# Optimization experiments

Hardware: AMD Instinct MI355X
Metric: run time of the kernel (lower is better)

The kernel has to match this reference:

```python
import jax, jax.numpy as jnp
import numpy as np

H = 256
V = 50257
L = 2048
B = 32


def setup_inputs() -> dict:
    key = jax.random.key(0)
    ks = jax.random.split(key, 14)
    s = 0.05  # weight scale
    return {
        "tokens": jax.random.randint(ks[0], (B,), 0, V),
        "hidden": jax.random.normal(ks[1], (1, B, H), jnp.float32),
        "cell": jax.random.normal(ks[2], (1, B, H), jnp.float32),
        "encoder_outputs": jax.random.normal(ks[3], (B, L, H), jnp.float32),
        "emb_table": jax.random.normal(ks[4], (V, H), jnp.float32) * s,
        "W_attn": jax.random.normal(ks[5], (H, 2 * H), jnp.float32) * s,
        "b_attn": jax.random.normal(ks[6], (H,), jnp.float32) * s,
        "v": jax.random.normal(ks[7], (H,), jnp.float32) * s,
        "W_ih": jax.random.normal(ks[8], (4 * H, 2 * H), jnp.float32) * s,
        "b_ih": jax.random.normal(ks[9], (4 * H,), jnp.float32) * s,
        "W_hh": jax.random.normal(ks[10], (4 * H, H), jnp.float32) * s,
        "b_hh": jax.random.normal(ks[11], (4 * H,), jnp.float32) * s,
        "W_out": jax.random.normal(ks[12], (V, 2 * H), jnp.float32) * s,
        "b_out": jax.random.normal(ks[13], (V,), jnp.float32) * s,
    }


def reference(tokens, hidden, cell, encoder_outputs, emb_table, W_attn, b_attn, v,
              W_ih, b_ih, W_hh, b_hh, W_out, b_out):
    # embedded: (B, H); dropout is identity in eval mode
    embedded = emb_table[tokens]
    h_last = hidden[-1]  # (B, H)

    # Bahdanau-style energy: attn(cat(h, e)) then dot with v (NO tanh, per source)
    # split the 2H-input linear into hidden part and encoder part
    Wh, We = W_attn[:, :H], W_attn[:, H:]
    eh = h_last @ Wh.T                                      # (B, H)
    ee = jnp.einsum('blh,kh->blk', encoder_outputs, We)     # (B, L, H)
    energy = eh[:, None, :] + ee + b_attn                   # (B, L, H)
    scores = energy @ v                                     # (B, L)
    attn_weights = jax.nn.softmax(scores, axis=-1)          # (B, L)

    # context = bmm(attn_weights, encoder_outputs)
    attn_applied = jnp.einsum('bl,blh->bh', attn_weights, encoder_outputs)  # (B, H)

    # single-step LSTM, input = cat(embedded, context): (B, 2H)
    x = jnp.concatenate([embedded, attn_applied], axis=-1)
    gates = x @ W_ih.T + b_ih + hidden[0] @ W_hh.T + b_hh   # (B, 4H)
    i_g, f_g, g_g, o_g = jnp.split(gates, 4, axis=-1)
    c_new = jax.nn.sigmoid(f_g) * cell[0] + jax.nn.sigmoid(i_g) * jnp.tanh(g_g)
    h_new = jax.nn.sigmoid(o_g) * jnp.tanh(c_new)           # (B, H)

    # output projection on cat(lstm_out, context): (B, 2H) -> (B, V)
    logits = jnp.concatenate([h_new, attn_applied], axis=-1) @ W_out.T + b_out
    log_probs = jax.nn.log_softmax(logits, axis=-1)

    return (log_probs, h_new[None], c_new[None], attn_weights[:, None, :])
```

## Files before the change

kernel.cpp:

```cpp
#include <hip/hip_runtime.h>
#include <cstddef>

#define H   256
#define L   2048
#define B   32
#define V   50257
#define H2  512
#define H4  1024
#define CH  64
#define NCH (L/CH)

#define LP_OFF 0
#define HN_OFF (B*V)
#define CN_OFF (HN_OFF + B*H)
#define AW_OFF (CN_OFF + B*H)

#define WS_XL    0
#define WS_S     (WS_XL + B*H2)
#define WS_AV    (WS_S + B*L)
#define WS_AM    (WS_AV + B*NCH*H)
#define WS_AZ    (WS_AM + B*NCH)
#define WS_PM    (WS_AZ + B*NCH)
#define WS_PZ    (WS_PM + 12800)

#define NBLK_LOG 393

typedef __attribute__((ext_vector_type(8))) short bf16x8;
typedef __attribute__((ext_vector_type(4))) float f32x4;

__device__ inline unsigned short f2bf(float f) {
    unsigned u = __builtin_bit_cast(unsigned, f);
    u += 0x7FFFu + ((u >> 16) & 1u);
    return (unsigned short)(u >> 16);
}

__global__ __launch_bounds__(256) void k_attn(const float* __restrict__ W_attn,
                                              const float* __restrict__ v,
                                              const float* __restrict__ enc,
                                              float* __restrict__ ws) {
    int bid = blockIdx.x;
    int b = bid >> 5, chunk = bid & (NCH - 1);
    int t = threadIdx.x;
    int wave = t >> 6, lane = t & 63;
    int g = lane >> 4, u = lane & 15;
    __shared__ float v_s[H];
    __shared__ float w_s[H];
    __shared__ float s_lds[CH];
    __shared__ float p_lds[CH];
    __shared__ float red[CH];
    __shared__ float vec_lds[4][256];

    v_s[t] = v[t];
    __syncthreads();
    {
        const float* base = W_attn + H + t;
        float wa = 0.f, wb = 0.f;
        #pragma unroll 8
        for (int k = 0; k < H; k += 2) {
            wa += v_s[k]     * base[(size_t)k * H2];
            wb += v_s[k + 1] * base[(size_t)(k + 1) * H2];
        }
        w_s[t] = wa + wb;
    }
    __syncthreads();

    size_t rowbase = (size_t)b * L + chunk * CH;
    const float4* w4s = (const float4*)w_s;
    float4 w0 = w4s[u], w1 = w4s[16 + u], w2 = w4s[32 + u], w3 = w4s[48 + u];

    #pragma unroll
    for (int ir = 0; ir < 4; ir++) {
        int rl = wave * 16 + ir * 4 + g;
        const float4* e4 = (const float4*)(enc + (rowbase + rl) * H);
        float4 a0 = e4[u], a1 = e4[16 + u], a2 = e4[32 + u], a3 = e4[48 + u];
        float p = a0.x * w0.x + a0.y * w0.y + a0.z * w0.z + a0.w * w0.w
                + a1.x * w1.x + a1.y * w1.y + a1.z * w1.z + a1.w * w1.w
                + a2.x * w2.x + a2.y * w2.y + a2.z * w2.z + a2.w * w2.w
                + a3.x * w3.x + a3.y * w3.y + a3.z * w3.z + a3.w * w3.w;
        p += __shfl_down(p, 8); p += __shfl_down(p, 4);
        p += __shfl_down(p, 2); p += __shfl_down(p, 1);
        if (u == 0) s_lds[rl] = p;
    }
    __syncthreads();

    if (t < CH) red[t] = s_lds[t];
    __syncthreads();
    for (int off = 32; off; off >>= 1) { if (t < off) red[t] = fmaxf(red[t], red[t + off]); __syncthreads(); }
    float m = red[0];
    __syncthreads();
    if (t < CH) {
        float e = __expf(s_lds[t] - m);
        p_lds[t] = e; red[t] = e;
        ws[WS_S + rowbase + t] = s_lds[t];
    }
    __syncthreads();
    for (int off = 32; off; off >>= 1) { if (t < off) red[t] += red[t + off]; __syncthreads(); }

    float4 acc = make_float4(0.f, 0.f, 0.f, 0.f);
    const float4* ebase = (const float4*)(enc + (rowbase + wave * 16) * H);
    #pragma unroll 4
    for (int i = 0; i < 16; i++) {
        float p = p_lds[wave * 16 + i];
        float4 a = ebase[i * 64 + lane];
        acc.x += p * a.x; acc.y += p * a.y; acc.z += p * a.z; acc.w += p * a.w;
    }
    *(float4*)&vec_lds[wave][lane * 4] = acc;
    __syncthreads();
    ws[WS_AV + (size_t)bid * 256 + t] = vec_lds[0][t] + vec_lds[1][t] + vec_lds[2][t] + vec_lds[3][t];
    if (t == 0) { ws[WS_AM + bid] = m; ws[WS_AZ + bid] = red[0]; }
}

__global__ __launch_bounds__(256) void k_fuse(const int* __restrict__ tokens,
                                              const float* __restrict__ emb,
                                              const float* __restrict__ hidden,
                                              const float* __restrict__ cell,
                                              const float* __restrict__ W_ih,
                                              const float* __restrict__ b_ih,
                                              const float* __restrict__ W_hh,
                                              const float* __restrict__ b_hh,
                                              float* __restrict__ ws,
                                              float* __restrict__ out) {
    int blk = blockIdx.x;
    int b = blk >> 4, s = blk & 15;
    int t = threadIdx.x;
    int wave = t >> 6, lane = t & 63;
    __shared__ float mc[NCH], zc[NCH];
    __shared__ float xs[H2];
    __shared__ float hs[H];
    __shared__ float gl[64];

    if (t < NCH) { mc[t] = ws[WS_AM + b * NCH + t]; zc[t] = ws[WS_AZ + b * NCH + t]; }
    hs[t] = hidden[(size_t)b * H + t];
    int tok = tokens[b];
    xs[t] = emb[(size_t)tok * H + t];
    __syncthreads();

    float M = -1e30f;
    #pragma unroll
    for (int c = 0; c < NCH; c++) M = fmaxf(M, mc[c]);
    float Z = 0.f;
    #pragma unroll
    for (int c = 0; c < NCH; c++) Z += zc[c] * __expf(mc[c] - M);
    float inv = 1.f / Z;
    float acc = 0.f;
    #pragma unroll 8
    for (int c = 0; c < NCH; c++) acc += __expf(mc[c] - M) * ws[WS_AV + (size_t)(b * NCH + c) * H + t];
    acc *= inv;
    xs[H + t] = acc;
    if (s == 0) {
        ws[WS_XL + b * H2 + H + t] = acc;
        #pragma unroll
        for (int j = 0; j < 8; j++) {
            int l = t + 256 * j;
            out[AW_OFF + (size_t)b * L + l] = __expf(ws[WS_S + (size_t)b * L + l] - M) * inv;
        }
    }
    __syncthreads();

    int ts = s * 16;
    const float4* xs4 = (const float4*)xs;
    const float4* hs4 = (const float4*)hs;
    float4 x0 = xs4[lane * 2], x1 = xs4[lane * 2 + 1];
    float4 xh = hs4[lane];
    for (int it = 0; it < 16; it++) {
        int j = (wave << 8) + ts + it;
        const float4* wi = (const float4*)(W_ih + (size_t)j * H2);
        float4 a0 = wi[lane * 2], a1 = wi[lane * 2 + 1];
        const float4* wh = (const float4*)(W_hh + (size_t)j * H);
        float4 a2 = wh[lane];
        float p = a0.x * x0.x + a0.y * x0.y + a0.z * x0.z + a0.w * x0.w
                + a1.x * x1.x + a1.y * x1.y + a1.z * x1.z + a1.w * x1.w
                + a2.x * xh.x + a2.y * xh.y + a2.z * xh.z + a2.w * xh.w;
        #pragma unroll
        for (int off = 32; off; off >>= 1) p += __shfl_down(p, off);
        if (lane == 0) gl[wave * 16 + it] = p + b_ih[j] + b_hh[j];
    }
    __syncthreads();

    if (t < 16) {
        int tt = ts + t;
        float ig = gl[t], fg = gl[16 + t], gg = gl[32 + t], og = gl[48 + t];
        float c = cell[(size_t)b * H + tt];
        float si = 1.f / (1.f + expf(-ig));
        float sf = 1.f / (1.f + expf(-fg));
        float so = 1.f / (1.f + expf(-og));
        float cn = sf * c + si * tanhf(gg);
        float hn = so * tanhf(cn);
        out[HN_OFF + b * H + tt] = hn;
        out[CN_OFF + b * H + tt] = cn;
        ws[WS_XL + b * H2 + tt] = hn;
    }
}

__global__ __launch_bounds__(256) void k_logits(const float* __restrict__ W_out,
                                                const float* __restrict__ b_out,
                                                float* __restrict__ ws,
                                                float* __restrict__ out) {
    __shared__ unsigned short Xl[32 * 520];
    int t = threadIdx.x;
    const float4* xl4 = (const float4*)(ws + WS_XL);
    #pragma unroll
    for (int it = 0; it < 16; it++) {
        int fi = t + 256 * it;
        int b = fi >> 7, kq = fi & 127;
        float4 xv = xl4[b * 128 + kq];
        unsigned p0 = (unsigned)f2bf(xv.x) | ((unsigned)f2bf(xv.y) << 16);
        unsigned p1 = (unsigned)f2bf(xv.z) | ((unsigned)f2bf(xv.w) << 16);
        unsigned* dst = (unsigned*)&Xl[b * 520 + kq * 4];
        dst[0] = p0; dst[1] = p1;
    }
    __syncthreads();

    int wave = t >> 6, lane = t & 63, quad = lane >> 4, m = lane & 15;
    int rbase = blockIdx.x * 128 + wave * 32;
    f32x4 zero4 = {0.f, 0.f, 0.f, 0.f};
    f32x4 acc[2][2];
    acc[0][0] = zero4; acc[0][1] = zero4; acc[1][0] = zero4; acc[1][1] = zero4;

    int r0 = rbase + m;
    int r1 = rbase + 16 + m;
    int r0c = r0 < V ? r0 : V - 1;
    int r1c = r1 < V ? r1 : V - 1;
    const float* wp0 = W_out + (size_t)r0c * H2 + quad * 8;
    const float* wp1 = W_out + (size_t)r1c * H2 + quad * 8;

    for (int kp = 0; kp < 16; kp++) {
        int k0 = kp * 32;
        float4 lo0 = *(const float4*)(wp0 + k0);
        float4 hi0 = *(const float4*)(wp0 + k0 + 4);
        float4 lo1 = *(const float4*)(wp1 + k0);
        float4 hi1 = *(const float4*)(wp1 + k0 + 4);
        bf16x8 a0, a1;
        a0[0]=(short)f2bf(lo0.x); a0[1]=(short)f2bf(lo0.y); a0[2]=(short)f2bf(lo0.z); a0[3]=(short)f2bf(lo0.w);
        a0[4]=(short)f2bf(hi0.x); a0[5]=(short)f2bf(hi0.y); a0[6]=(short)f2bf(hi0.z); a0[7]=(short)f2bf(hi0.w);
        a1[0]=(short)f2bf(lo1.x); a1[1]=(short)f2bf(lo1.y); a1[2]=(short)f2bf(lo1.z); a1[3]=(short)f2bf(lo1.w);
        a1[4]=(short)f2bf(hi1.x); a1[5]=(short)f2bf(hi1.y); a1[6]=(short)f2bf(hi1.z); a1[7]=(short)f2bf(hi1.w);
        bf16x8 b0 = *(bf16x8*)&Xl[(size_t)m * 520 + k0 + quad * 8];
        bf16x8 b1 = *(bf16x8*)&Xl[(size_t)(16 + m) * 520 + k0 + quad * 8];
        acc[0][0] = __builtin_amdgcn_mfma_f32_16x16x32_bf16(a0, b0, acc[0][0], 0, 0, 0);
        acc[0][1] = __builtin_amdgcn_mfma_f32_16x16x32_bf16(a0, b1, acc[0][1], 0, 0, 0);
        acc[1][0] = __builtin_amdgcn_mfma_f32_16x16x32_bf16(a1, b0, acc[1][0], 0, 0, 0);
        acc[1][1] = __builtin_amdgcn_mfma_f32_16x16x32_bf16(a1, b1, acc[1][1], 0, 0, 0);
    }

    float val[2][2][4];
    #pragma unroll
    for (int s = 0; s < 2; s++) {
        #pragma unroll
        for (int i = 0; i < 4; i++) {
            int rr = rbase + s * 16 + quad * 4 + i;
            float bo = (rr < V) ? b_out[rr] : 0.f;
            #pragma unroll
            for (int nt = 0; nt < 2; nt++) {
                float vv = acc[s][nt][i] + bo;
                if (rr < V) {
                    int bcol = nt * 16 + m;
                    out[(size_t)bcol * V + rr] = vv;
                    val[s][nt][i] = vv;
                } else {
                    val[s][nt][i] = -1e30f;
                }
            }
        }
    }
    float pm[2], pz[2];
    #pragma unroll
    for (int nt = 0; nt < 2; nt++) {
        float mx = -1e30f;
        #pragma unroll
        for (int s = 0; s < 2; s++)
            #pragma unroll
            for (int i = 0; i < 4; i++) mx = fmaxf(mx, val[s][nt][i]);
        float sm = 0.f;
        #pragma unroll
        for (int s = 0; s < 2; s++)
            #pragma unroll
            for (int i = 0; i < 4; i++) sm += __expf(val[s][nt][i] - mx);
        pm[nt] = mx; pz[nt] = sm;
    }
    #pragma unroll
    for (int off = 16; off <= 32; off <<= 1) {
        #pragma unroll
        for (int nt = 0; nt < 2; nt++) {
            float om = __shfl_xor(pm[nt], off);
            float oz = __shfl_xor(pz[nt], off);
            float nm = fmaxf(pm[nt], om);
            pz[nt] = pz[nt] * __expf(pm[nt] - nm) + oz * __expf(om - nm);
            pm[nt] = nm;
        }
    }
    __syncthreads();
    float* red = (float*)Xl;
    if (quad == 0) {
        #pragma unroll
        for (int nt = 0; nt < 2; nt++) {
            red[wave * 32 + nt * 16 + m]       = pm[nt];
            red[128 + wave * 32 + nt * 16 + m] = pz[nt];
        }
    }
    __syncthreads();
    if (t < 32) {
        float mf = -1e30f;
        #pragma unroll
        for (int w = 0; w < 4; w++) mf = fmaxf(mf, red[w * 32 + t]);
        float z = 0.f;
        #pragma unroll
        for (int w = 0; w < 4; w++) z += red[128 + w * 32 + t] * __expf(red[w * 32 + t] - mf);
        ws[WS_PM + t * 400 + blockIdx.x] = mf;
        ws[WS_PZ + t * 400 + blockIdx.x] = z;
    }
}

__global__ __launch_bounds__(256) void k_lsm_final(const float* __restrict__ ws,
                                                   float* __restrict__ out) {
    int b = blockIdx.y, t = threadIdx.x;
    __shared__ float rm[256], rz[256];
    float m = -1e30f, z = 0.f;
    for (int i = t; i < NBLK_LOG; i += 256) {
        float mi = ws[WS_PM + b * 400 + i];
        float zi = ws[WS_PZ + b * 400 + i];
        float nm = fmaxf(m, mi);
        z = z * __expf(m - nm) + zi * __expf(mi - nm);
        m = nm;
    }
    rm[t] = m; rz[t] = z; __syncthreads();
    for (int off = 128; off; off >>= 1) {
        if (t < off) {
            float m2 = rm[t + off], z2 = rz[t + off];
            float nm = fmaxf(rm[t], m2);
            rz[t] = rz[t] * __expf(rm[t] - nm) + z2 * __expf(m2 - nm);
            rm[t] = nm;
        }
        __syncthreads();
    }
    float M = rm[0], LZ = logf(rz[0]);
    int rbase = blockIdx.x * 1024 + t;
    #pragma unroll
    for (int j = 0; j < 4; j++) {
        int r = rbase + 256 * j;
        if (r < V) {
            size_t i = (size_t)b * V + r;
            out[i] = out[i] - M - LZ;
        }
    }
}

extern "C" void kernel_launch(void* const* d_in, const int* in_sizes, int n_in,
                              void* d_out, int out_size, void* d_ws, size_t ws_size,
                              hipStream_t stream) {
    const int*   tokens = (const int*)d_in[0];
    const float* hidden = (const float*)d_in[1];
    const float* cell   = (const float*)d_in[2];
    const float* enc    = (const float*)d_in[3];
    const float* emb    = (const float*)d_in[4];
    const float* W_attn = (const float*)d_in[5];
    const float* v      = (const float*)d_in[7];
    const float* W_ih   = (const float*)d_in[8];
    const float* b_ih   = (const float*)d_in[9];
    const float* W_hh   = (const float*)d_in[10];
    const float* b_hh   = (const float*)d_in[11];
    const float* W_out  = (const float*)d_in[12];
    const float* b_out  = (const float*)d_in[13];
    float* out = (float*)d_out;
    float* ws  = (float*)d_ws;

    k_attn<<<B * NCH, 256, 0, stream>>>(W_attn, v, enc, ws);
    k_fuse<<<B * 16, 256, 0, stream>>>(tokens, emb, hidden, cell, W_ih, b_ih, W_hh, b_hh, ws, out);
    k_logits<<<NBLK_LOG, 256, 0, stream>>>(W_out, b_out, ws, out);
    k_lsm_final<<<dim3((V + 1023) / 1024, B), 256, 0, stream>>>(ws, out);
}
```

Measured before the change: 297.2 us.

## Merge four kernels into one cooperative persistent kernel with grid syncs

Replaces the separate attention, LSTM, logits and log-softmax kernels with a single cooperative kernel of 512 blocks that runs each phase and separates them with grid.sync. Work is remapped so each block handles multiple attention chunks and logits tiles (now 64-row tiles with a one-step software prefetch of W_out). The goal is to remove per-launch overhead and inter-kernel gaps, at the cost of grid-wide barrier latency and reduced per-phase parallelism. A fallback launches the same kernel four times if the cooperative launch fails.

```diff
diff --git a/kernel.cpp b/kernel.cpp
--- a/kernel.cpp
+++ b/kernel.cpp
@@ -1,5 +1,8 @@
 #include <hip/hip_runtime.h>
+#include <hip/hip_cooperative_groups.h>
 #include <cstddef>
+
+namespace cg = cooperative_groups;
 
 #define H   256
 #define L   2048
@@ -21,9 +24,10 @@
 #define WS_AM    (WS_AV + B*NCH*H)
 #define WS_AZ    (WS_AM + B*NCH)
 #define WS_PM    (WS_AZ + B*NCH)
-#define WS_PZ    (WS_PM + 12800)
-
-#define NBLK_LOG 393
+#define WS_PZ    (WS_PM + 32*800)
+
+#define NT_LOG 786
+#define NBLK   512
 
 typedef __attribute__((ext_vector_type(8))) short bf16x8;
 typedef __attribute__((ext_vector_type(4))) float f32x4;
@@ -34,313 +38,302 @@
     return (unsigned short)(u >> 16);
 }
 
-__global__ __launch_bounds__(256) void k_attn(const float* __restrict__ W_attn,
-                                              const float* __restrict__ v,
-                                              const float* __restrict__ enc,
-                                              float* __restrict__ ws) {
-    int bid = blockIdx.x;
-    int b = bid >> 5, chunk = bid & (NCH - 1);
-    int t = threadIdx.x;
+__global__ __launch_bounds__(256, 2) void k_mega(
+    int p_lo, int p_hi,
+    const int*   __restrict__ tokens, const float* __restrict__ emb,
+    const float* __restrict__ hidden, const float* __restrict__ cell,
+    const float* __restrict__ enc,    const float* __restrict__ W_attn,
+    const float* __restrict__ v,      const float* __restrict__ W_ih,
+    const float* __restrict__ b_ih,   const float* __restrict__ W_hh,
+    const float* __restrict__ b_hh,   const float* __restrict__ W_out,
+    const float* __restrict__ b_out,  float* __restrict__ ws,
+    float* __restrict__ out)
+{
+    __shared__ __align__(16) float smf[8576];
+    cg::grid_group grid = cg::this_grid();
+    int blk = blockIdx.x, t = threadIdx.x;
     int wave = t >> 6, lane = t & 63;
-    int g = lane >> 4, u = lane & 15;
-    __shared__ float v_s[H];
-    __shared__ float w_s[H];
-    __shared__ float s_lds[CH];
-    __shared__ float p_lds[CH];
-    __shared__ float red[CH];
-    __shared__ float vec_lds[4][256];
-
-    v_s[t] = v[t];
-    __syncthreads();
-    {
-        const float* base = W_attn + H + t;
-        float wa = 0.f, wb = 0.f;
+
+    if (p_lo <= 0 && 0 <= p_hi) {
+        float* v_s   = smf;
+        float* w_s   = smf + 256;
+        float* s_lds = smf + 512;
+        float* p_lds = smf + 576;
+        float* red   = smf + 640;
+        float* vec   = smf + 704;
+        int g = lane >> 4, u = lane & 15;
+
+        v_s[t] = v[t];
+        __syncthreads();
+        {
+            const float* base = W_attn + H + t;
+            float wa = 0.f, wb = 0.f;
+            #pragma unroll 8
+            for (int k = 0; k < H; k += 2) {
+                wa += v_s[k]     * base[(size_t)k * H2];
+                wb += v_s[k + 1] * base[(size_t)(k + 1) * H2];
+            }
+            w_s[t] = wa + wb;
+        }
+        __syncthreads();
+        const float4* w4s = (const float4*)w_s;
+        float4 w0 = w4s[u], w1 = w4s[16 + u], w2 = w4s[32 + u], w3 = w4s[48 + u];
+
+        for (int pass = 0; pass < 2; pass++) {
+            int bid = blk + pass * NBLK;
+            int b = bid >> 5, chunk = bid & (NCH - 1);
+            size_t rowbase = (size_t)b * L + chunk * CH;
+
+            #pragma unroll
+            for (int ir = 0; ir < 4; ir++) {
+                int rl = wave * 16 + ir * 4 + g;
+                const float4* e4 = (const float4*)(enc + (rowbase + rl) * H);
+                float4 a0 = e4[u], a1 = e4[16 + u], a2 = e4[32 + u], a3 = e4[48 + u];
+                float p = a0.x * w0.x + a0.y * w0.y + a0.z * w0.z + a0.w * w0.w
+                        + a1.x * w1.x + a1.y * w1.y + a1.z * w1.z + a1.w * w1.w
+                        + a2.x * w2.x + a2.y * w2.y + a2.z * w2.z + a2.w * w2.w
+                        + a3.x * w3.x + a3.y * w3.y + a3.z * w3.z + a3.w * w3.w;
+                p += __shfl_down(p, 8); p += __shfl_down(p, 4);
+                p += __shfl_down(p, 2); p += __shfl_down(p, 1);
+                if (u == 0) s_lds[rl] = p;
+            }
+            __syncthreads();
+
+            if (t < CH) red[t] = s_lds[t];
+            __syncthreads();
+            for (int off = 32; off; off >>= 1) { if (t < off) red[t] = fmaxf(red[t], red[t + off]); __syncthreads(); }
+            float m = red[0];
+            __syncthreads();
+            if (t < CH) {
+                float e = __expf(s_lds[t] - m);
+                p_lds[t] = e; red[t] = e;
+                ws[WS_S + rowbase + t] = s_lds[t];
+            }
+            __syncthreads();
+            for (int off = 32; off; off >>= 1) { if (t < off) red[t] += red[t + off]; __syncthreads(); }
+
+            float4 acc = make_float4(0.f, 0.f, 0.f, 0.f);
+            const float4* ebase = (const float4*)(enc + (rowbase + wave * 16) * H);
+            #pragma unroll 4
+            for (int i = 0; i < 16; i++) {
+                float p = p_lds[wave * 16 + i];
+                float4 a = ebase[i * 64 + lane];
+                acc.x += p * a.x; acc.y += p * a.y; acc.z += p * a.z; acc.w += p * a.w;
+            }
+            *(float4*)&vec[wave * 256 + lane * 4] = acc;
+            __syncthreads();
+            ws[WS_AV + (size_t)bid * 256 + t] = vec[t] + vec[256 + t] + vec[512 + t] + vec[768 + t];
+            if (t == 0) { ws[WS_AM + bid] = m; ws[WS_AZ + bid] = red[0]; }
+            __syncthreads();
+        }
+    }
+    if (p_lo <= 0 && 1 <= p_hi) grid.sync();
+
+    if (p_lo <= 1 && 1 <= p_hi) {
+        int b = blk >> 4, s = blk & 15;
+        float* mc = smf;
+        float* zc = smf + 32;
+        float* xs = smf + 64;
+        float* hs = smf + 576;
+        float* gl = smf + 832;
+
+        if (t < NCH) { mc[t] = ws[WS_AM + b * NCH + t]; zc[t] = ws[WS_AZ + b * NCH + t]; }
+        hs[t] = hidden[(size_t)b * H + t];
+        xs[t] = emb[(size_t)tokens[b] * H + t];
+        __syncthreads();
+
+        float M = -1e30f;
+        #pragma unroll
+        for (int c = 0; c < NCH; c++) M = fmaxf(M, mc[c]);
+        float Z = 0.f;
+        #pragma unroll
+        for (int c = 0; c < NCH; c++) Z += zc[c] * __expf(mc[c] - M);
+        float inv = 1.f / Z;
+        float acc = 0.f;
         #pragma unroll 8
-        for (int k = 0; k < H; k += 2) {
-            wa += v_s[k]     * base[(size_t)k * H2];
-            wb += v_s[k + 1] * base[(size_t)(k + 1) * H2];
-        }
-        w_s[t] = wa + wb;
-    }
-    __syncthreads();
-
-    size_t rowbase = (size_t)b * L + chunk * CH;
-    const float4* w4s = (const float4*)w_s;
-    float4 w0 = w4s[u], w1 = w4s[16 + u], w2 = w4s[32 + u], w3 = w4s[48 + u];
-
-    #pragma unroll
-    for (int ir = 0; ir < 4; ir++) {
-        int rl = wave * 16 + ir * 4 + g;
-        const float4* e4 = (const float4*)(enc + (rowbase + rl) * H);
-        float4 a0 = e4[u], a1 = e4[16 + u], a2 = e4[32 + u], a3 = e4[48 + u];
-        float p = a0.x * w0.x + a0.y * w0.y + a0.z * w0.z + a0.w * w0.w
-                + a1.x * w1.x + a1.y * w1.y + a1.z * w1.z + a1.w * w1.w
-                + a2.x * w2.x + a2.y * w2.y + a2.z * w2.z + a2.w * w2.w
-                + a3.x * w3.x + a3.y * w3.y + a3.z * w3.z + a3.w * w3.w;
-        p += __shfl_down(p, 8); p += __shfl_down(p, 4);
-        p += __shfl_down(p, 2); p += __shfl_down(p, 1);
-        if (u == 0) s_lds[rl] = p;
-    }
-    __syncthreads();
-
-    if (t < CH) red[t] = s_lds[t];
-    __syncthreads();
-    for (int off = 32; off; off >>= 1) { if (t < off) red[t] = fmaxf(red[t], red[t + off]); __syncthreads(); }
-    float m = red[0];
-    __syncthreads();
-    if (t < CH) {
-        float e = __expf(s_lds[t] - m);
-        p_lds[t] = e; red[t] = e;
-        ws[WS_S + rowbase + t] = s_lds[t];
-    }
-    __syncthreads();
-    for (int off = 32; off; off >>= 1) { if (t < off) red[t] += red[t + off]; __syncthreads(); }
-
-    float4 acc = make_float4(0.f, 0.f, 0.f, 0.f);
-    const float4* ebase = (const float4*)(enc + (rowbase + wave * 16) * H);
-    #pragma unroll 4
-    for (int i = 0; i < 16; i++) {
-        float p = p_lds[wave * 16 + i];
-        float4 a = ebase[i * 64 + lane];
-        acc.x += p * a.x; acc.y += p * a.y; acc.z += p * a.z; acc.w += p * a.w;
-    }
-    *(float4*)&vec_lds[wave][lane * 4] = acc;
-    __syncthreads();
-    ws[WS_AV + (size_t)bid * 256 + t] = vec_lds[0][t] + vec_lds[1][t] + vec_lds[2][t] + vec_lds[3][t];
-    if (t == 0) { ws[WS_AM + bid] = m; ws[WS_AZ + bid] = red[0]; }
-}
-
-__global__ __launch_bounds__(256) void k_fuse(const int* __restrict__ tokens,
-                                              const float* __restrict__ emb,
-                                              const float* __restrict__ hidden,
-                                              const float* __restrict__ cell,
-                                              const float* __restrict__ W_ih,
-                                              const float* __restrict__ b_ih,
-                                              const float* __restrict__ W_hh,
-                                              const float* __restrict__ b_hh,
-                                              float* __restrict__ ws,
-                                              float* __restrict__ out) {
-    int blk = blockIdx.x;
-    int b = blk >> 4, s = blk & 15;
-    int t = threadIdx.x;
-    int wave = t >> 6, lane = t & 63;
-    __shared__ float mc[NCH], zc[NCH];
-    __shared__ float xs[H2];
-    __shared__ float hs[H];
-    __shared__ float gl[64];
-
-    if (t < NCH) { mc[t] = ws[WS_AM + b * NCH + t]; zc[t] = ws[WS_AZ + b * NCH + t]; }
-    hs[t] = hidden[(size_t)b * H + t];
-    int tok = tokens[b];
-    xs[t] = emb[(size_t)tok * H + t];
-    __syncthreads();
-
-    float M = -1e30f;
-    #pragma unroll
-    for (int c = 0; c < NCH; c++) M = fmaxf(M, mc[c]);
-    float Z = 0.f;
-    #pragma unroll
-    for (int c = 0; c < NCH; c++) Z += zc[c] * __expf(mc[c] - M);
-    float inv = 1.f / Z;
-    float acc = 0.f;
-    #pragma unroll 8
-    for (int c = 0; c < NCH; c++) acc += __expf(mc[c] - M) * ws[WS_AV + (size_t)(b * NCH + c) * H + t];
-    acc *= inv;
-    xs[H + t] = acc;
-    if (s == 0) {
-        ws[WS_XL + b * H2 + H + t] = acc;
+        for (int c = 0; c < NCH; c++) acc += __expf(mc[c] - M) * ws[WS_AV + (size_t)(b * NCH + c) * H + t];
+        acc *= inv;
+        xs[H + t] = acc;
+        if (s == 0) {
+            ws[WS_XL + b * H2 + H + t] = acc;
+            #pragma unroll
+            for (int j = 0; j < 8; j++) {
+                int l = t + 256 * j;
+                out[AW_OFF + (size_t)b * L + l] = __expf(ws[WS_S + (size_t)b * L + l] - M) * inv;
+            }
+        }
+        __syncthreads();
+
+        int ts = s * 16;
+        const float4* xs4 = (const float4*)xs;
+        const float4* hs4 = (const float4*)hs;
+        float4 x0 = xs4[lane * 2], x1 = xs4[lane * 2 + 1];
+        float4 xh = hs4[lane];
+        for (int it = 0; it < 16; it++) {
+            int j = (wave << 8) + ts + it;
+            const float4* wi = (const float4*)(W_ih + (size_t)j * H2);
+            float4 a0 = wi[lane * 2], a1 = wi[lane * 2 + 1];
+            const float4* wh = (const float4*)(W_hh + (size_t)j * H);
+            float4 a2 = wh[lane];
+            float p = a0.x * x0.x + a0.y * x0.y + a0.z * x0.z + a0.w * x0.w
+                    + a1.x * x1.x + a1.y * x1.y + a1.z * x1.z + a1.w * x1.w
+                    + a2.x * xh.x + a2.y * xh.y + a2.z * xh.z + a2.w * xh.w;
+            #pragma unroll
+            for (int off = 32; off; off >>= 1) p += __shfl_down(p, off);
+            if (lane == 0) gl[wave * 16 + it] = p + b_ih[j] + b_hh[j];
+        }
+        __syncthreads();
+
+        if (t < 16) {
+            int tt = ts + t;
+            float ig = gl[t], fg = gl[16 + t], gg = gl[32 + t], og = gl[48 + t];
+            float c = cell[(size_t)b * H + tt];
+            float si = 1.f / (1.f + expf(-ig));
+            float sf = 1.f / (1.f + expf(-fg));
+            float so = 1.f / (1.f + expf(-og));
+            float cn = sf * c + si * tanhf(gg);
+            float hn = so * tanhf(cn);
+            out[HN_OFF + b * H + tt] = hn;
+            out[CN_OFF + b * H + tt] = cn;
+            ws[WS_XL + b * H2 + tt] = hn;
+        }
+    }
+    if (p_lo <= 1 && 2 <= p_hi) grid.sync();
+
+    if (p_lo <= 2 && 2 <= p_hi) {
+        unsigned short* Xl = (unsigned short*)smf;
+        float* red2 = smf + 8320;
+        const float4* xl4 = (const float4*)(ws + WS_XL);
         #pragma unroll
-        for (int j = 0; j < 8; j++) {
-            int l = t + 256 * j;
-            out[AW_OFF + (size_t)b * L + l] = __expf(ws[WS_S + (size_t)b * L + l] - M) * inv;
-        }
-    }
-    __syncthreads();
-
-    int ts = s * 16;
-    const float4* xs4 = (const float4*)xs;
-    const float4* hs4 = (const float4*)hs;
-    float4 x0 = xs4[lane * 2], x1 = xs4[lane * 2 + 1];
-    float4 xh = hs4[lane];
-    for (int it = 0; it < 16; it++) {
-        int j = (wave << 8) + ts + it;
-        const float4* wi = (const float4*)(W_ih + (size_t)j * H2);
-        float4 a0 = wi[lane * 2], a1 = wi[lane * 2 + 1];
-        const float4* wh = (const float4*)(W_hh + (size_t)j * H);
-        float4 a2 = wh[lane];
-        float p = a0.x * x0.x + a0.y * x0.y + a0.z * x0.z + a0.w * x0.w
-                + a1.x * x1.x + a1.y * x1.y + a1.z * x1.z + a1.w * x1.w
-                + a2.x * xh.x + a2.y * xh.y + a2.z * xh.z + a2.w * xh.w;
-        #pragma unroll
-        for (int off = 32; off; off >>= 1) p += __shfl_down(p, off);
-        if (lane == 0) gl[wave * 16 + it] = p + b_ih[j] + b_hh[j];
-    }
-    __syncthreads();
-
-    if (t < 16) {
-        int tt = ts + t;
-        float ig = gl[t], fg = gl[16 + t], gg = gl[32 + t], og = gl[48 + t];
-        float c = cell[(size_t)b * H + tt];
-        float si = 1.f / (1.f + expf(-ig));
-        float sf = 1.f / (1.f + expf(-fg));
-        float so = 1.f / (1.f + expf(-og));
-        float cn = sf * c + si * tanhf(gg);
-        float hn = so * tanhf(cn);
-        out[HN_OFF + b * H + tt] = hn;
-        out[CN_OFF + b * H + tt] = cn;
-        ws[WS_XL + b * H2 + tt] = hn;
-    }
-}
-
-__global__ __launch_bounds__(256) void k_logits(const float* __restrict__ W_out,
-                                                const float* __restrict__ b_out,
-                                                float* __restrict__ ws,
-                                                float* __restrict__ out) {
-    __shared__ unsigned short Xl[32 * 520];
-    int t = threadIdx.x;
-    const float4* xl4 = (const float4*)(ws + WS_XL);
-    #pragma unroll
-    for (int it = 0; it < 16; it++) {
-        int fi = t + 256 * it;
-        int b = fi >> 7, kq = fi & 127;
-        float4 xv = xl4[b * 128 + kq];
-        unsigned p0 = (unsigned)f2bf(xv.x) | ((unsigned)f2bf(xv.y) << 16);
-        unsigned p1 = (unsigned)f2bf(xv.z) | ((unsigned)f2bf(xv.w) << 16);
-        unsigned* dst = (unsigned*)&Xl[b * 520 + kq * 4];
-        dst[0] = p0; dst[1] = p1;
-    }
-    __syncthreads();
-
-    int wave = t >> 6, lane = t & 63, quad = lane >> 4, m = lane & 15;
-    int rbase = blockIdx.x * 128 + wave * 32;
-    f32x4 zero4 = {0.f, 0.f, 0.f, 0.f};
-    f32x4 acc[2][2];
-    acc[0][0] = zero4; acc[0][1] = zero4; acc[1][0] = zero4; acc[1][1] = zero4;
-
-    int r0 = rbase + m;
-    int r1 = rbase + 16 + m;
-    int r0c = r0 < V ? r0 : V - 1;
-    int r1c = r1 < V ? r1 : V - 1;
-    const float* wp0 = W_out + (size_t)r0c * H2 + quad * 8;
-    const float* wp1 = W_out + (size_t)r1c * H2 + quad * 8;
-
-    for (int kp = 0; kp < 16; kp++) {
-        int k0 = kp * 32;
-        float4 lo0 = *(const float4*)(wp0 + k0);
-        float4 hi0 = *(const float4*)(wp0 + k0 + 4);
-        float4 lo1 = *(const float4*)(wp1 + k0);
-        float4 hi1 = *(const float4*)(wp1 + k0 + 4);
-        bf16x8 a0, a1;
-        a0[0]=(short)f2bf(lo0.x); a0[1]=(short)f2bf(lo0.y); a0[2]=(short)f2bf(lo0.z); a0[3]=(short)f2bf(lo0.w);
-        a0[4]=(short)f2bf(hi0.x); a0[5]=(short)f2bf(hi0.y); a0[6]=(short)f2bf(hi0.z); a0[7]=(short)f2bf(hi0.w);
-        a1[0]=(short)f2bf(lo1.x); a1[1]=(short)f2bf(lo1.y); a1[2]=(short)f2bf(lo1.z); a1[3]=(short)f2bf(lo1.w);
-        a1[4]=(short)f2bf(hi1.x); a1[5]=(short)f2bf(hi1.y); a1[6]=(short)f2bf(hi1.z); a1[7]=(short)f2bf(hi1.w);
-        bf16x8 b0 = *(bf16x8*)&Xl[(size_t)m * 520 + k0 + quad * 8];
-        bf16x8 b1 = *(bf16x8*)&Xl[(size_t)(16 + m) * 520 + k0 + quad * 8];
-        acc[0][0] = __builtin_amdgcn_mfma_f32_16x16x32_bf16(a0, b0, acc[0][0], 0, 0, 0);
-        acc[0][1] = __builtin_amdgcn_mfma_f32_16x16x32_bf16(a0, b1, acc[0][1], 0, 0, 0);
-        acc[1][0] = __builtin_amdgcn_mfma_f32_16x16x32_bf16(a1, b0, acc[1][0], 0, 0, 0);
-        acc[1][1] = __builtin_amdgcn_mfma_f32_16x16x32_bf16(a1, b1, acc[1][1], 0, 0, 0);
-    }
-
-    float val[2][2][4];
-    #pragma unroll
-    for (int s = 0; s < 2; s++) {
-        #pragma unroll
-        for (int i = 0; i < 4; i++) {
-            int rr = rbase + s * 16 + quad * 4 + i;
-            float bo = (rr < V) ? b_out[rr] : 0.f;
+        for (int it = 0; it < 16; it++) {
+            int fi = t + 256 * it;
+            int bb = fi >> 7, kq = fi & 127;
+            float4 xv = xl4[bb * 128 + kq];
+            unsigned p0 = (unsigned)f2bf(xv.x) | ((unsigned)f2bf(xv.y) << 16);
+            unsigned p1 = (unsigned)f2bf(xv.z) | ((unsigned)f2bf(xv.w) << 16);
+            unsigned* dst = (unsigned*)&Xl[bb * 520 + kq * 4];
+            dst[0] = p0; dst[1] = p1;
+        }
+        __syncthreads();
+
+        int quad = lane >> 4, m = lane & 15;
+        for (int tile = blk; tile < NT_LOG; tile += NBLK) {
+            int rbase = tile * 64 + wave * 16;
+            int r0 = rbase + m;
+            int rc = r0 < V ? r0 : V - 1;
+            const float* wp = W_out + (size_t)rc * H2 + quad * 8;
+            f32x4 acc0 = {0.f, 0.f, 0.f, 0.f}, acc1 = {0.f, 0.f, 0.f, 0.f};
+
+            float4 lo = *(const float4*)(wp);
+            float4 hi = *(const float4*)(wp + 4);
+            #pragma unroll
+            for (int kp = 0; kp < 16; kp++) {
+                int k0 = kp * 32;
+                float4 nlo, nhi;
+                if (kp < 15) {
+                    nlo = *(const float4*)(wp + k0 + 32);
+                    nhi = *(const float4*)(wp + k0 + 36);
+                }
+                bf16x8 a;
+                a[0]=(short)f2bf(lo.x); a[1]=(short)f2bf(lo.y); a[2]=(short)f2bf(lo.z); a[3]=(short)f2bf(lo.w);
+                a[4]=(short)f2bf(hi.x); a[5]=(short)f2bf(hi.y); a[6]=(short)f2bf(hi.z); a[7]=(short)f2bf(hi.w);
+                bf16x8 b0 = *(bf16x8*)&Xl[(size_t)m * 520 + k0 + quad * 8];
+                bf16x8 b1 = *(bf16x8*)&Xl[(size_t)(16 + m) * 520 + k0 + quad * 8];
+                acc0 = __builtin_amdgcn_mfma_f32_16x16x32_bf16(a, b0, acc0, 0, 0, 0);
+                acc1 = __builtin_amdgcn_mfma_f32_16x16x32_bf16(a, b1, acc1, 0, 0, 0);
+                lo = nlo; hi = nhi;
+            }
+
+            float val[2][4];
+            #pragma unroll
+            for (int i = 0; i < 4; i++) {
+                int rr = rbase + quad * 4 + i;
+                float bo = (rr < V) ? b_out[rr] : 0.f;
+                float v0 = acc0[i] + bo, v1 = acc1[i] + bo;
+                if (rr < V) {
+                    out[(size_t)m * V + rr]        = v0;
+                    out[(size_t)(16 + m) * V + rr] = v1;
+                    val[0][i] = v0; val[1][i] = v1;
+                } else { val[0][i] = -1e30f; val[1][i] = -1e30f; }
+            }
+            float pm[2], pz[2];
             #pragma unroll
             for (int nt = 0; nt < 2; nt++) {
-                float vv = acc[s][nt][i] + bo;
-                if (rr < V) {
-                    int bcol = nt * 16 + m;
-                    out[(size_t)bcol * V + rr] = vv;
-                    val[s][nt][i] = vv;
-                } else {
-                    val[s][nt][i] = -1e30f;
-                }
-            }
-        }
-    }
-    float pm[2], pz[2];
-    #pragma unroll
-    for (int nt = 0; nt < 2; nt++) {
-        float mx = -1e30f;
-        #pragma unroll
-        for (int s = 0; s < 2; s++)
-            #pragma unroll
-            for (int i = 0; i < 4; i++) mx = fmaxf(mx, val[s][nt][i]);
-        float sm = 0.f;
-        #pragma unroll
-        for (int s = 0; s < 2; s++)
-            #pragma unroll
-            for (int i = 0; i < 4; i++) sm += __expf(val[s][nt][i] - mx);
-        pm[nt] = mx; pz[nt] = sm;
-    }
-    #pragma unroll
-    for (int off = 16; off <= 32; off <<= 1) {
-        #pragma unroll
-        for (int nt = 0; nt < 2; nt++) {
-            float om = __shfl_xor(pm[nt], off);
-            float oz = __shfl_xor(pz[nt], off);
-            float nm = fmaxf(pm[nt], om);
-            pz[nt] = pz[nt] * __expf(pm[nt] - nm) + oz * __expf(om - nm);
-            pm[nt] = nm;
-        }
-    }
-    __syncthreads();
-    float* red = (float*)Xl;
-    if (quad == 0) {
-        #pragma unroll
-        for (int nt = 0; nt < 2; nt++) {
-            red[wave * 32 + nt * 16 + m]       = pm[nt];
-            red[128 + wave * 32 + nt * 16 + m] = pz[nt];
-        }
-    }
-    __syncthreads();
-    if (t < 32) {
-        float mf = -1e30f;
-        #pragma unroll
-        for (int w = 0; w < 4; w++) mf = fmaxf(mf, red[w * 32 + t]);
-        float z = 0.f;
-        #pragma unroll
-        for (int w = 0; w < 4; w++) z += red[128 + w * 32 + t] * __expf(red[w * 32 + t] - mf);
-        ws[WS_PM + t * 400 + blockIdx.x] = mf;
-        ws[WS_PZ + t * 400 + blockIdx.x] = z;
-    }
-}
-
-__global__ __launch_bounds__(256) void k_lsm_final(const float* __restrict__ ws,
-                                                   float* __restrict__ out) {
-    int b = blockIdx.y, t = threadIdx.x;
-    __shared__ float rm[256], rz[256];
-    float m = -1e30f, z = 0.f;
-    for (int i = t; i < NBLK_LOG; i += 256) {
-        float mi = ws[WS_PM + b * 400 + i];
-        float zi = ws[WS_PZ + b * 400 + i];
-        float nm = fmaxf(m, mi);
-        z = z * __expf(m - nm) + zi * __expf(mi - nm);
-        m = nm;
-    }
-    rm[t] = m; rz[t] = z; __syncthreads();
-    for (int off = 128; off; off >>= 1) {
-        if (t < off) {
-            float m2 = rm[t + off], z2 = rz[t + off];
-            float nm = fmaxf(rm[t], m2);
-            rz[t] = rz[t] * __expf(rm[t] - nm) + z2 * __expf(m2 - nm);
-            rm[t] = nm;
-        }
-        __syncthreads();
-    }
-    float M = rm[0], LZ = logf(rz[0]);
-    int rbase = blockIdx.x * 1024 + t;
-    #pragma unroll
-    for (int j = 0; j < 4; j++) {
-        int r = rbase + 256 * j;
-        if (r < V) {
-            size_t i = (size_t)b * V + r;
-            out[i] = out[i] - M - LZ;
+                float mx = -1e30f;
+                #pragma unroll
+                for (int i = 0; i < 4; i++) mx = fmaxf(mx, val[nt][i]);
+                float sm = 0.f;
+                #pragma unroll
+                for (int i = 0; i < 4; i++) sm += __expf(val[nt][i] - mx);
+                pm[nt] = mx; pz[nt] = sm;
+            }
+            #pragma unroll
+            for (int off = 16; off <= 32; off <<= 1) {
+                #pragma unroll
+                for (int nt = 0; nt < 2; nt++) {
+                    float om = __shfl_xor(pm[nt], off);
+                    float oz = __shfl_xor(pz[nt], off);
+                    float nm = fmaxf(pm[nt], om);
+                    pz[nt] = pz[nt] * __expf(pm[nt] - nm) + oz * __expf(om - nm);
+                    pm[nt] = nm;
+                }
+            }
+            __syncthreads();
+            if (quad == 0) {
+                #pragma unroll
+                for (int nt = 0; nt < 2; nt++) {
+                    red2[wave * 32 + nt * 16 + m]       = pm[nt];
+                    red2[128 + wave * 32 + nt * 16 + m] = pz[nt];
+                }
+            }
+            __syncthreads();
+            if (t < 32) {
+                float mf = -1e30f;
+                #pragma unroll
+                for (int w = 0; w < 4; w++) mf = fmaxf(mf, red2[w * 32 + t]);
+                float z = 0.f;
+                #pragma unroll
+                for (int w = 0; w < 4; w++) z += red2[128 + w * 32 + t] * __expf(red2[w * 32 + t] - mf);
+                ws[WS_PM + t * 800 + tile] = mf;
+                ws[WS_PZ + t * 800 + tile] = z;
+            }
+        }
+    }
+    if (p_lo <= 2 && 3 <= p_hi) grid.sync();
+
+    if (p_lo <= 3 && 3 <= p_hi) {
+        if (blk < 416) {
+            int b = blk / 13, ch = blk - b * 13;
+            float* rm = smf;
+            float* rz = smf + 256;
+            float m = -1e30f, z = 0.f;
+            for (int i = t; i < NT_LOG; i += 256) {
+                float mi = ws[WS_PM + b * 800 + i];
+                float zi = ws[WS_PZ + b * 800 + i];
+                float nm = fmaxf(m, mi);
+                z = z * __expf(m - nm) + zi * __expf(mi - nm);
+                m = nm;
+            }
+            rm[t] = m; rz[t] = z; __syncthreads();
+            for (int off = 128; off; off >>= 1) {
+                if (t < off) {
+                    float m2 = rm[t + off], z2 = rz[t + off];
+                    float nm = fmaxf(rm[t], m2);
+                    rz[t] = rz[t] * __expf(rm[t] - nm) + z2 * __expf(m2 - nm);
+                    rm[t] = nm;
+                }
+                __syncthreads();
+            }
+            float MM = rm[0], LZ = logf(rz[0]);
+            int rb = ch * 4096 + t;
+            #pragma unroll
+            for (int j = 0; j < 16; j++) {
+                int r = rb + 256 * j;
+                if (r < V) {
+                    size_t i = (size_t)b * V + r;
+                    out[i] = out[i] - MM - LZ;
+                }
+            }
         }
     }
 }
@@ -364,8 +357,15 @@
     float* out = (float*)d_out;
     float* ws  = (float*)d_ws;
 
-    k_attn<<<B * NCH, 256, 0, stream>>>(W_attn, v, enc, ws);
-    k_fuse<<<B * 16, 256, 0, stream>>>(tokens, emb, hidden, cell, W_ih, b_ih, W_hh, b_hh, ws, out);
-    k_logits<<<NBLK_LOG, 256, 0, stream>>>(W_out, b_out, ws, out);
-    k_lsm_final<<<dim3((V + 1023) / 1024, B), 256, 0, stream>>>(ws, out);
+    int p_lo = 0, p_hi = 3;
+    void* args[] = { &p_lo, &p_hi, &tokens, &emb, &hidden, &cell, &enc, &W_attn,
+                     &v, &W_ih, &b_ih, &W_hh, &b_hh, &W_out, &b_out, &ws, &out };
+    hipError_t e = hipLaunchCooperativeKernel((const void*)k_mega, dim3(NBLK), dim3(256),
+                                              args, 0, stream);
+    if (e != hipSuccess) {
+        for (int p = 0; p < 4; p++) {
+            k_mega<<<NBLK, 256, 0, stream>>>(p, p, tokens, emb, hidden, cell, enc, W_attn,
+                                             v, W_ih, b_ih, W_hh, b_hh, W_out, b_out, ws, out);
+        }
+    }
 }
```

Result: slower. 489.9 us (+64.8%).

## Halve logits tile per block and software-prefetch W_out rows three steps ahead

Applied to the files above, without the earlier changes.

The logits kernel now gives each wave 16 vocabulary rows instead of 32, which doubles the grid to 786 blocks. A register-level prefetch pipeline loads W_out three k-steps ahead so the bf16 conversion and MFMA overlap with memory latency. It also adds a launch-bounds occupancy hint, a separate LDS reduction buffer, and full unrolling of the attention accumulation loop. The partial-softmax workspace stride widens to match the larger grid, at the cost of more partials for the final reduction and higher register pressure from the prefetch buffers.

```diff
diff --git a/kernel.cpp b/kernel.cpp
--- a/kernel.cpp
+++ b/kernel.cpp
@@ -21,9 +21,9 @@
 #define WS_AM    (WS_AV + B*NCH*H)
 #define WS_AZ    (WS_AM + B*NCH)
 #define WS_PM    (WS_AZ + B*NCH)
-#define WS_PZ    (WS_PM + 12800)
-
-#define NBLK_LOG 393
+#define WS_PZ    (WS_PM + 32*800)
+
+#define NT_LOG 786
 
 typedef __attribute__((ext_vector_type(8))) short bf16x8;
 typedef __attribute__((ext_vector_type(4))) float f32x4;
@@ -98,7 +98,7 @@
 
     float4 acc = make_float4(0.f, 0.f, 0.f, 0.f);
     const float4* ebase = (const float4*)(enc + (rowbase + wave * 16) * H);
-    #pragma unroll 4
+    #pragma unroll
     for (int i = 0; i < 16; i++) {
         float p = p_lds[wave * 16 + i];
         float4 a = ebase[i * 64 + lane];
@@ -131,8 +131,7 @@
 
     if (t < NCH) { mc[t] = ws[WS_AM + b * NCH + t]; zc[t] = ws[WS_AZ + b * NCH + t]; }
     hs[t] = hidden[(size_t)b * H + t];
-    int tok = tokens[b];
-    xs[t] = emb[(size_t)tok * H + t];
+    xs[t] = emb[(size_t)tokens[b] * H + t];
     __syncthreads();
 
     float M = -1e30f;
@@ -192,90 +191,73 @@
     }
 }
 
-__global__ __launch_bounds__(256) void k_logits(const float* __restrict__ W_out,
-                                                const float* __restrict__ b_out,
-                                                float* __restrict__ ws,
-                                                float* __restrict__ out) {
+__global__ __launch_bounds__(256, 4) void k_logits(const float* __restrict__ W_out,
+                                                   const float* __restrict__ b_out,
+                                                   float* __restrict__ ws,
+                                                   float* __restrict__ out) {
     __shared__ unsigned short Xl[32 * 520];
+    __shared__ float red2[256];
     int t = threadIdx.x;
     const float4* xl4 = (const float4*)(ws + WS_XL);
     #pragma unroll
     for (int it = 0; it < 16; it++) {
         int fi = t + 256 * it;
-        int b = fi >> 7, kq = fi & 127;
-        float4 xv = xl4[b * 128 + kq];
+        int bb = fi >> 7, kq = fi & 127;
+        float4 xv = xl4[bb * 128 + kq];
         unsigned p0 = (unsigned)f2bf(xv.x) | ((unsigned)f2bf(xv.y) << 16);
         unsigned p1 = (unsigned)f2bf(xv.z) | ((unsigned)f2bf(xv.w) << 16);
-        unsigned* dst = (unsigned*)&Xl[b * 520 + kq * 4];
+        unsigned* dst = (unsigned*)&Xl[bb * 520 + kq * 4];
         dst[0] = p0; dst[1] = p1;
     }
     __syncthreads();
 
     int wave = t >> 6, lane = t & 63, quad = lane >> 4, m = lane & 15;
-    int rbase = blockIdx.x * 128 + wave * 32;
-    f32x4 zero4 = {0.f, 0.f, 0.f, 0.f};
-    f32x4 acc[2][2];
-    acc[0][0] = zero4; acc[0][1] = zero4; acc[1][0] = zero4; acc[1][1] = zero4;
-
+    int rbase = blockIdx.x * 64 + wave * 16;
     int r0 = rbase + m;
-    int r1 = rbase + 16 + m;
-    int r0c = r0 < V ? r0 : V - 1;
-    int r1c = r1 < V ? r1 : V - 1;
-    const float* wp0 = W_out + (size_t)r0c * H2 + quad * 8;
-    const float* wp1 = W_out + (size_t)r1c * H2 + quad * 8;
-
+    int rc = r0 < V ? r0 : V - 1;
+    const float4* wq = (const float4*)(W_out + (size_t)rc * H2 + quad * 8);
+
+    f32x4 acc0 = {0.f, 0.f, 0.f, 0.f}, acc1 = {0.f, 0.f, 0.f, 0.f};
+
+    float4 pl0 = wq[0],  ph0 = wq[1];
+    float4 pl1 = wq[8],  ph1 = wq[9];
+    float4 pl2 = wq[16], ph2 = wq[17];
+    #pragma unroll
     for (int kp = 0; kp < 16; kp++) {
         int k0 = kp * 32;
-        float4 lo0 = *(const float4*)(wp0 + k0);
-        float4 hi0 = *(const float4*)(wp0 + k0 + 4);
-        float4 lo1 = *(const float4*)(wp1 + k0);
-        float4 hi1 = *(const float4*)(wp1 + k0 + 4);
-        bf16x8 a0, a1;
-        a0[0]=(short)f2bf(lo0.x); a0[1]=(short)f2bf(lo0.y); a0[2]=(short)f2bf(lo0.z); a0[3]=(short)f2bf(lo0.w);
-        a0[4]=(short)f2bf(hi0.x); a0[5]=(short)f2bf(hi0.y); a0[6]=(short)f2bf(hi0.z); a0[7]=(short)f2bf(hi0.w);
-        a1[0]=(short)f2bf(lo1.x); a1[1]=(short)f2bf(lo1.y); a1[2]=(short)f2bf(lo1.z); a1[3]=(short)f2bf(lo1.w);
-        a1[4]=(short)f2bf(hi1.x); a1[5]=(short)f2bf(hi1.y); a1[6]=(short)f2bf(hi1.z); a1[7]=(short)f2bf(hi1.w);
+        bf16x8 a;
+        a[0]=(short)f2bf(pl0.x); a[1]=(short)f2bf(pl0.y); a[2]=(short)f2bf(pl0.z); a[3]=(short)f2bf(pl0.w);
+        a[4]=(short)f2bf(ph0.x); a[5]=(short)f2bf(ph0.y); a[6]=(short)f2bf(ph0.z); a[7]=(short)f2bf(ph0.w);
         bf16x8 b0 = *(bf16x8*)&Xl[(size_t)m * 520 + k0 + quad * 8];
         bf16x8 b1 = *(bf16x8*)&Xl[(size_t)(16 + m) * 520 + k0 + quad * 8];
-        acc[0][0] = __builtin_amdgcn_mfma_f32_16x16x32_bf16(a0, b0, acc[0][0], 0, 0, 0);
-        acc[0][1] = __builtin_amdgcn_mfma_f32_16x16x32_bf16(a0, b1, acc[0][1], 0, 0, 0);
-        acc[1][0] = __builtin_amdgcn_mfma_f32_16x16x32_bf16(a1, b0, acc[1][0], 0, 0, 0);
-        acc[1][1] = __builtin_amdgcn_mfma_f32_16x16x32_bf16(a1, b1, acc[1][1], 0, 0, 0);
-    }
-
-    float val[2][2][4];
-    #pragma unroll
-    for (int s = 0; s < 2; s++) {
-        #pragma unroll
-        for (int i = 0; i < 4; i++) {
-            int rr = rbase + s * 16 + quad * 4 + i;
-            float bo = (rr < V) ? b_out[rr] : 0.f;
-            #pragma unroll
-            for (int nt = 0; nt < 2; nt++) {
-                float vv = acc[s][nt][i] + bo;
-                if (rr < V) {
-                    int bcol = nt * 16 + m;
-                    out[(size_t)bcol * V + rr] = vv;
-                    val[s][nt][i] = vv;
-                } else {
-                    val[s][nt][i] = -1e30f;
-                }
-            }
-        }
+        acc0 = __builtin_amdgcn_mfma_f32_16x16x32_bf16(a, b0, acc0, 0, 0, 0);
+        acc1 = __builtin_amdgcn_mfma_f32_16x16x32_bf16(a, b1, acc1, 0, 0, 0);
+        pl0 = pl1; ph0 = ph1;
+        pl1 = pl2; ph1 = ph2;
+        if (kp < 13) { pl2 = wq[(kp + 3) * 8]; ph2 = wq[(kp + 3) * 8 + 1]; }
+    }
+
+    float val[2][4];
+    #pragma unroll
+    for (int i = 0; i < 4; i++) {
+        int rr = rbase + quad * 4 + i;
+        float bo = (rr < V) ? b_out[rr] : 0.f;
+        float v0 = acc0[i] + bo, v1 = acc1[i] + bo;
+        if (rr < V) {
+            out[(size_t)m * V + rr]        = v0;
+            out[(size_t)(16 + m) * V + rr] = v1;
+            val[0][i] = v0; val[1][i] = v1;
+        } else { val[0][i] = -1e30f; val[1][i] = -1e30f; }
     }
     float pm[2], pz[2];
     #pragma unroll
     for (int nt = 0; nt < 2; nt++) {
         float mx = -1e30f;
         #pragma unroll
-        for (int s = 0; s < 2; s++)
-            #pragma unroll
-            for (int i = 0; i < 4; i++) mx = fmaxf(mx, val[s][nt][i]);
+        for (int i = 0; i < 4; i++) mx = fmaxf(mx, val[nt][i]);
         float sm = 0.f;
         #pragma unroll
-        for (int s = 0; s < 2; s++)
-            #pragma unroll
-            for (int i = 0; i < 4; i++) sm += __expf(val[s][nt][i] - mx);
+        for (int i = 0; i < 4; i++) sm += __expf(val[nt][i] - mx);
         pm[nt] = mx; pz[nt] = sm;
     }
     #pragma unroll
@@ -290,24 +272,23 @@
         }
     }
     __syncthreads();
-    float* red = (float*)Xl;
     if (quad == 0) {
         #pragma unroll
         for (int nt = 0; nt < 2; nt++) {
-            red[wave * 32 + nt * 16 + m]       = pm[nt];
-            red[128 + wave * 32 + nt * 16 + m] = pz[nt];
+            red2[wave * 32 + nt * 16 + m]       = pm[nt];
+            red2[128 + wave * 32 + nt * 16 + m] = pz[nt];
         }
     }
     __syncthreads();
     if (t < 32) {
         float mf = -1e30f;
         #pragma unroll
-        for (int w = 0; w < 4; w++) mf = fmaxf(mf, red[w * 32 + t]);
+        for (int w = 0; w < 4; w++) mf = fmaxf(mf, red2[w * 32 + t]);
         float z = 0.f;
         #pragma unroll
-        for (int w = 0; w < 4; w++) z += red[128 + w * 32 + t] * __expf(red[w * 32 + t] - mf);
-        ws[WS_PM + t * 400 + blockIdx.x] = mf;
-        ws[WS_PZ + t * 400 + blockIdx.x] = z;
+        for (int w = 0; w < 4; w++) z += red2[128 + w * 32 + t] * __expf(red2[w * 32 + t] - mf);
+        ws[WS_PM + t * 800 + blockIdx.x] = mf;
+        ws[WS_PZ + t * 800 + blockIdx.x] = z;
     }
 }
 
@@ -316,9 +297,9 @@
     int b = blockIdx.y, t = threadIdx.x;
     __shared__ float rm[256], rz[256];
     float m = -1e30f, z = 0.f;
-    for (int i = t; i < NBLK_LOG; i += 256) {
-        float mi = ws[WS_PM + b * 400 + i];
-        float zi = ws[WS_PZ + b * 400 + i];
+    for (int i = t; i < NT_LOG; i += 256) {
+        float mi = ws[WS_PM + b * 800 + i];
+        float zi = ws[WS_PZ + b * 800 + i];
         float nm = fmaxf(m, mi);
         z = z * __expf(m - nm) + zi * __expf(mi - nm);
         m = nm;
@@ -366,6 +347,6 @@
 
     k_attn<<<B * NCH, 256, 0, stream>>>(W_attn, v, enc, ws);
     k_fuse<<<B * 16, 256, 0, stream>>>(tokens, emb, hidden, cell, W_ih, b_ih, W_hh, b_hh, ws, out);
-    k_logits<<<NBLK_LOG, 256, 0, stream>>>(W_out, b_out, ws, out);
+    k_logits<<<NT_LOG, 256, 0, stream>>>(W_out, b_out, ws, out);
     k_lsm_final<<<dim3((V + 1023) / 1024, B), 256, 0, stream>>>(ws, out);
 }
```

Result: no change. 303.0 us (+1.9%).
